# Optimization experiments

Measured on AMD Instinct MI355X. Metric: run time of the kernel, lower is better.

Reference implementation:

```python
import jax, jax.numpy as jnp
import numpy as np

N_EMBD = 1024
N_HEAD = 16
B, T = 8, 1024

def setup_inputs() -> dict:
    key = jax.random.key(0)
    ks = jax.random.split(key, 5)
    s = 0.02
    return {
        'x': jax.random.normal(ks[0], (B, T, N_EMBD), dtype=jnp.float32),
        'w_attn': jax.random.normal(ks[1], (N_EMBD, 3 * N_EMBD), dtype=jnp.float32) * s,
        'b_attn': jax.random.normal(ks[2], (3 * N_EMBD,), dtype=jnp.float32) * s,
        'w_proj': jax.random.normal(ks[3], (N_EMBD, N_EMBD), dtype=jnp.float32) * s,
        'b_proj': jax.random.normal(ks[4], (N_EMBD,), dtype=jnp.float32) * s,
    }

def reference(x, w_attn, b_attn, w_proj, b_proj):
    Bb, Tt, C = x.shape
    hd = C // N_HEAD  # head dim
    qkv = x @ w_attn + b_attn                      # [B,T,3C]
    q, k, v = jnp.split(qkv, 3, axis=2)
    # [B,T,C] -> [B,H,T,hd]
    def to_heads(t):
        return t.reshape(Bb, Tt, N_HEAD, hd).transpose(0, 2, 1, 3)
    q, k, v = to_heads(q), to_heads(k), to_heads(v)
    scale = 1.0 / jnp.sqrt(jnp.asarray(hd, dtype=x.dtype))
    att = jnp.einsum('bhqd,bhkd->bhqk', q, k) * scale  # [B,H,T,T]
    causal = jnp.tril(jnp.ones((Tt, Tt), dtype=bool))  # [T,T]
    att = jnp.where(causal[None, None, :, :], att, -jnp.inf)
    att = jax.nn.softmax(att, axis=-1)
    y = jnp.einsum('bhqk,bhkd->bhqd', att, v)          # [B,H,T,hd]
    y = y.transpose(0, 2, 1, 3).reshape(Bb, Tt, C)
    y = y @ w_proj + b_proj
    return y
```

## Files before the change

kernel.cpp:

```cpp
#include <hip/hip_runtime.h>
#include <stdint.h>

#define N_EMBD 1024
#define NHEAD  16
#define HDIM   64
#define BATCH  8
#define SEQ    1024
#define MROWS  (BATCH*SEQ)

typedef __bf16 bf16x8 __attribute__((ext_vector_type(8)));
typedef float  f32x4  __attribute__((ext_vector_type(4)));

__device__ inline unsigned short f2bf(float f) {
  uint32_t u = __float_as_uint(f);
  u += 0x7FFFu + ((u >> 16) & 1u);
  return (unsigned short)(u >> 16);
}

__device__ inline f32x4 mfma_bf16(bf16x8 a, bf16x8 b, f32x4 c) {
  return __builtin_amdgcn_mfma_f32_16x16x32_bf16(a, b, c, 0, 0, 0);
}

__device__ inline void gload_lds16(const unsigned short* g, unsigned short* l) {
  __builtin_amdgcn_global_load_lds(
      (const __attribute__((address_space(1))) void*)g,
      (__attribute__((address_space(3))) void*)l,
      16, 0, 0);
}

#define DSB __builtin_amdgcn_sched_barrier(0)
#define BARRIER __builtin_amdgcn_s_barrier()
#define VMC(n) asm volatile("s_waitcnt vmcnt(" #n ")" ::: "memory")
#define LGKM0 asm volatile("s_waitcnt lgkmcnt(0)" ::: "memory"); DSB

__global__ __launch_bounds__(256) void cast_f32_bf16(
    const float* __restrict__ in, unsigned short* __restrict__ out, int n) {
  int i = (blockIdx.x * 256 + threadIdx.x) * 4;
  if (i >= n) return;
  float4 v = *(const float4*)(in + i);
  ushort4 o;
  o.x = f2bf(v.x); o.y = f2bf(v.y); o.z = f2bf(v.z); o.w = f2bf(v.w);
  *(ushort4*)(out + i) = o;
}

__global__ __launch_bounds__(256) void transpose_cast2(
    const float* __restrict__ wa, unsigned short* __restrict__ oa,
    const float* __restrict__ wp, unsigned short* __restrict__ op) {
  __shared__ unsigned short tile[64 * 72];
  const int K = 1024;
  int bx = blockIdx.x;
  const float* in; unsigned short* out; int N;
  if (bx < 48) { in = wa; out = oa; N = 3072; }
  else         { in = wp; out = op; N = 1024; bx -= 48; }
  int k0 = blockIdx.y * 64, n0 = bx * 64;
  int t = threadIdx.x;
  {
    int col = (t & 15) * 4;
#pragma unroll
    for (int it = 0; it < 4; ++it) {
      int row = (t >> 4) + it * 16;
      float4 v = *(const float4*)(in + (size_t)(k0 + row) * N + n0 + col);
      ushort4 o;
      o.x = f2bf(v.x); o.y = f2bf(v.y); o.z = f2bf(v.z); o.w = f2bf(v.w);
      *(ushort4*)&tile[row * 72 + col] = o;
    }
  }
  __syncthreads();
  {
    int kcol = (t & 7) * 8;
#pragma unroll
    for (int it = 0; it < 2; ++it) {
      int nrow = (t >> 3) + it * 32;
      alignas(16) unsigned short tmp[8];
#pragma unroll
      for (int j = 0; j < 8; ++j) tmp[j] = tile[(kcol + j) * 72 + nrow];
      *(uint4*)(out + (size_t)(n0 + nrow) * K + k0 + kcol) = *(const uint4*)tmp;
    }
  }
}

#define GEMM98_BODY(A_, Bt_)                                                    \
  __shared__ unsigned short Asl[2][8192];                                       \
  __shared__ unsigned short Bsl[2][8192];                                       \
  const int tid = threadIdx.x;                                                  \
  const int l = tid & 63, w = tid >> 6;                                         \
  const int wr = w >> 1, wc = w & 1;                                            \
  const int g = l >> 4, fr = l & 15;                                            \
  f32x4 acc[4][4];                                                              \
  _Pragma("unroll") for (int i = 0; i < 4; ++i)                                 \
    _Pragma("unroll") for (int j = 0; j < 4; ++j)                               \
      _Pragma("unroll") for (int r = 0; r < 4; ++r) acc[i][j][r] = 0.0f;        \
  const int rr = tid >> 3;                                                      \
  const int cs = ((tid & 7) * 16) ^ ((rr & 7) << 4);                            \
  const char* srcA[4]; const char* srcB[4];                                     \
  _Pragma("unroll") for (int c = 0; c < 4; ++c) {                               \
    srcA[c] = (const char*)(A_) + (size_t)(m0 + c * 32 + rr) * 2048 + cs;       \
    srcB[c] = (const char*)(Bt_) + (size_t)(n0 + c * 32 + rr) * 2048 + cs;      \
  }                                                                             \
  const int ldso = tid * 8;                                         \
  const int arow = (wr * 64 + fr) * 128;                                        \
  const int brow = (wc * 64 + fr) * 128;                                        \
  int colk[2];                                                                  \
  colk[0] = (g * 16) ^ ((fr & 7) << 4);                                         \
  colk[1] = (64 + g * 16) ^ ((fr & 7) << 4);                                    \
  _Pragma("unroll") for (int c = 0; c < 4; ++c)                                 \
    gload_lds16((const unsigned short*)(srcA[c]), &Asl[0][ldso + c * 2048]);    \
  _Pragma("unroll") for (int c = 0; c < 4; ++c)                                 \
    gload_lds16((const unsigned short*)(srcB[c]), &Bsl[0][ldso + c * 2048]);    \
  _Pragma("unroll") for (int c = 0; c < 4; ++c)                                 \
    gload_lds16((const unsigned short*)(srcA[c] + 128), &Asl[1][ldso + c * 2048]);\
  _Pragma("unroll") for (int c = 0; c < 4; ++c)                                 \
    gload_lds16((const unsigned short*)(srcB[c] + 128), &Bsl[1][ldso + c * 2048]);\
  for (int kt = 0; kt < 16; ++kt) {                                             \
    const int cur = kt & 1;                                                     \
    if (kt < 15) { VMC(8); } else { VMC(0); }                                   \
    DSB; BARRIER; DSB;                                                          \
    _Pragma("unroll") for (int ks = 0; ks < 2; ++ks) {                          \
      bf16x8 av[4], bv[4];                                                      \
      _Pragma("unroll") for (int m = 0; m < 4; ++m)                             \
        av[m] = *(const bf16x8*)((const char*)&Asl[cur][0] + arow +             \
                                 m * 16 * 128 + colk[ks]);                      \
      _Pragma("unroll") for (int n = 0; n < 4; ++n)                             \
        bv[n] = *(const bf16x8*)((const char*)&Bsl[cur][0] + brow +             \
                                 n * 16 * 128 + colk[ks]);                      \
      _Pragma("unroll") for (int n = 0; n < 4; ++n)                             \
        _Pragma("unroll") for (int m = 0; m < 4; ++m)                           \
          acc[m][n] = mfma_bf16(av[m], bv[n], acc[m][n]);                       \
    }                                                                           \
    LGKM0; BARRIER; DSB;                                                        \
    if (kt < 14) {                                                              \
      const int ko = (kt + 2) * 128;                                            \
      _Pragma("unroll") for (int c = 0; c < 4; ++c)                             \
        gload_lds16((const unsigned short*)(srcA[c] + ko),                      \
                    &Asl[cur][ldso + c * 2048]);                                \
      _Pragma("unroll") for (int c = 0; c < 4; ++c)                             \
        gload_lds16((const unsigned short*)(srcB[c] + ko),                      \
                    &Bsl[cur][ldso + c * 2048]);                                \
    }                                                                           \
  }

__global__ __launch_bounds__(256) void gemm_qkv(
    const unsigned short* __restrict__ A, const unsigned short* __restrict__ Bt,
    const float* __restrict__ bias,
    unsigned short* __restrict__ Qo, unsigned short* __restrict__ Ko,
    unsigned short* __restrict__ VTo) {
  const int bid = blockIdx.x;
  const int xcd = bid & 7;
  const int local = bid >> 3;
  const int nchunk = local >> 6;
  const int rem = local & 63;
  const int m0 = (xcd * 8 + (rem >> 3)) * 128;
  const int n0 = (nchunk * 8 + (rem & 7)) * 128;
  GEMM98_BODY(A, Bt)
#pragma unroll
  for (int i = 0; i < 4; ++i) {
    int mb = m0 + wr * 64 + i * 16 + 4 * g;
    int bidx = mb >> 10;
    int t = mb & 1023;
#pragma unroll
    for (int j = 0; j < 4; ++j) {
      int n = n0 + wc * 64 + j * 16 + fr;
      float bv2 = bias[n];
      int part = n >> 10;
      int nn2 = n & 1023;
      int h = nn2 >> 6, d = nn2 & 63;
      if (part == 2) {
        alignas(8) unsigned short pk[4];
#pragma unroll
        for (int r = 0; r < 4; ++r) pk[r] = f2bf(acc[i][j][r] + bv2);
        *(ushort4*)&VTo[((size_t)(bidx * NHEAD + h) * HDIM + d) * SEQ + t] =
            *(const ushort4*)pk;
      } else {
        unsigned short* dst = (part == 0) ? Qo : Ko;
        float scl = (part == 0) ? 0.125f : 1.0f;
        size_t base = ((size_t)(bidx * NHEAD + h) * SEQ + t) * HDIM + d;
#pragma unroll
        for (int r = 0; r < 4; ++r)
          dst[base + (size_t)r * HDIM] = f2bf((acc[i][j][r] + bv2) * scl);
      }
    }
  }
}

__global__ __launch_bounds__(256) void gemm_proj(
    const unsigned short* __restrict__ A, const unsigned short* __restrict__ Bt,
    const float* __restrict__ bias, float* __restrict__ Out) {
  const int bid = blockIdx.x;
  const int xcd = bid & 7;
  const int local = bid >> 3;
  const int m0 = (xcd * 8 + (local >> 3)) * 128;
  const int n0 = (local & 7) * 128;
  GEMM98_BODY(A, Bt)
#pragma unroll
  for (int i = 0; i < 4; ++i) {
    int mb = m0 + wr * 64 + i * 16 + 4 * g;
#pragma unroll
    for (int j = 0; j < 4; ++j) {
      int n = n0 + wc * 64 + j * 16 + fr;
      float bv2 = bias[n];
#pragma unroll
      for (int r = 0; r < 4; ++r)
        Out[(size_t)(mb + r) * N_EMBD + n] = acc[i][j][r] + bv2;
    }
  }
}

__global__ __launch_bounds__(256) void attn_kernel(
    const unsigned short* __restrict__ Q, const unsigned short* __restrict__ Kv,
    const unsigned short* __restrict__ VT, unsigned short* __restrict__ Y) {
  __shared__ unsigned short Kt[2][4096];
  __shared__ unsigned short Vt[2][4096];
  __shared__ unsigned short p_lds[4 * 32 * 72];
  __shared__ float smx[4][32];
  int tid = threadIdx.x, l = tid & 63, w = tid >> 6;
  int bid = blockIdx.x;
  int swz = (bid & 7) * 64 + (bid >> 3);
  int bh = swz >> 2;
  int pairIdx = swz & 3;
  int b = bh >> 4, h = bh & 15;
  const unsigned short* Qb = Q + (size_t)bh * SEQ * HDIM;
  const char* Kc = (const char*)(Kv + (size_t)bh * SEQ * HDIM);
  const char* Vc = (const char*)(VT + (size_t)bh * HDIM * SEQ);
  unsigned short* pw = &p_lds[w * 32 * 72];
  const int g = l >> 4;
  const int fr = l & 15;

  const int P0 = tid * 16, P1 = tid * 16 + 4096;
  const int r0 = P0 >> 7, r1 = P1 >> 7;
  const int s0 = (P0 & 127) ^ ((r0 & 7) << 4);
  const int s1 = (P1 & 127) ^ ((r1 & 7) << 4);
  const char* Kg0 = Kc + r0 * 128 + s0;
  const char* Kg1 = Kc + r1 * 128 + s1;
  const char* Vg0 = Vc + (size_t)r0 * 2048 + s0;
  const char* Vg1 = Vc + (size_t)r1 * 2048 + s1;

  const int bc = (16 * g) ^ ((l & 7) << 4);

  for (int part = 0; part < 2; ++part) {
    const int qt = (part == 0) ? pairIdx : 7 - pairIdx;
    const int q0 = qt * 128;
    const int wq = q0 + w * 32;

    bf16x8 aq[2][2];
#pragma unroll
    for (int i = 0; i < 2; ++i)
#pragma unroll
      for (int ik = 0; ik < 2; ++ik)
        aq[i][ik] = *(const bf16x8*)&Qb[(size_t)(wq + i * 16 + fr) * HDIM + ik * 32 + 8 * g];

    float mrun[2], lpart[2];
    mrun[0] = mrun[1] = 0.0f;
    lpart[0] = lpart[1] = 0.0f;
    f32x4 acc_o[2][4];
#pragma unroll
    for (int i = 0; i < 2; ++i)
#pragma unroll
      for (int jd = 0; jd < 4; ++jd)
#pragma unroll
        for (int r = 0; r < 4; ++r) acc_o[i][jd][r] = 0.0f;

    const int n_it = (q0 + 128) >> 6;

    gload_lds16((const unsigned short*)(Kg0), &Kt[0][P0 >> 1]);
    gload_lds16((const unsigned short*)(Kg1), &Kt[0][P1 >> 1]);
    gload_lds16((const unsigned short*)(Vg0), &Vt[0][P0 >> 1]);
    gload_lds16((const unsigned short*)(Vg1), &Vt[0][P1 >> 1]);

    for (int it = 0; it < n_it; ++it) {
      const int kv0 = it << 6;
      const int cur = it & 1;
      if (it + 1 < n_it) {
        const int nx = kv0 + 64;
        gload_lds16((const unsigned short*)(Kg0 + nx * 128), &Kt[cur ^ 1][P0 >> 1]);
        gload_lds16((const unsigned short*)(Kg1 + nx * 128), &Kt[cur ^ 1][P1 >> 1]);
        gload_lds16((const unsigned short*)(Vg0 + nx * 2),   &Vt[cur ^ 1][P0 >> 1]);
        gload_lds16((const unsigned short*)(Vg1 + nx * 2),   &Vt[cur ^ 1][P1 >> 1]);
        VMC(4);
      } else {
        VMC(0);
      }
      DSB; BARRIER; DSB;

      const char* Kbuf = (const char*)Kt[cur];
      const char* Vbuf = (const char*)Vt[cur];

      f32x4 s2[2][4];
#pragma unroll
      for (int i = 0; i < 2; ++i)
#pragma unroll
        for (int j = 0; j < 4; ++j)
#pragma unroll
          for (int r = 0; r < 4; ++r) s2[i][j][r] = 0.0f;

      __builtin_amdgcn_s_setprio(1);
#pragma unroll
      for (int ik = 0; ik < 2; ++ik) {
#pragma unroll
        for (int j = 0; j < 4; ++j) {
          bf16x8 bk = *(const bf16x8*)(Kbuf + (j * 16 + fr) * 128 + (bc ^ (ik << 6)));
#pragma unroll
          for (int i = 0; i < 2; ++i) s2[i][j] = mfma_bf16(bk, aq[i][ik], s2[i][j]);
        }
      }
      __builtin_amdgcn_s_setprio(0);

      bool need_mask = (kv0 + 63) > wq;
      if (need_mask) {
#pragma unroll
        for (int i = 0; i < 2; ++i) {
          int q = wq + i * 16 + fr;
#pragma unroll
          for (int j = 0; j < 4; ++j)
#pragma unroll
            for (int r = 0; r < 4; ++r) {
              int kv = kv0 + j * 16 + 4 * g + r;
              if (kv > q) s2[i][j][r] = -3.0e38f;
            }
        }
      }

      float pmloc[2];
#pragma unroll
      for (int i = 0; i < 2; ++i) {
        float m01 = fmaxf(fmaxf(s2[i][0][0], s2[i][0][1]), fmaxf(s2[i][0][2], s2[i][0][3]));
        float m11 = fmaxf(fmaxf(s2[i][1][0], s2[i][1][1]), fmaxf(s2[i][1][2], s2[i][1][3]));
        float m21 = fmaxf(fmaxf(s2[i][2][0], s2[i][2][1]), fmaxf(s2[i][2][2], s2[i][2][3]));
        float m31 = fmaxf(fmaxf(s2[i][3][0], s2[i][3][1]), fmaxf(s2[i][3][2], s2[i][3][3]));
        pmloc[i] = fmaxf(fmaxf(m01, m11), fmaxf(m21, m31));
      }
      bool ok = (pmloc[0] <= mrun[0] + 8.0f) && (pmloc[1] <= mrun[1] + 8.0f);
      if (!__all(ok)) {
#pragma unroll
        for (int i = 0; i < 2; ++i) {
          float mm = pmloc[i];
          mm = fmaxf(mm, __shfl_xor(mm, 16, 64));
          mm = fmaxf(mm, __shfl_xor(mm, 32, 64));
          float mn = fmaxf(mrun[i], mm);
          float sc = __expf(mrun[i] - mn);
          mrun[i] = mn;
          lpart[i] *= sc;
          if (g == 0) smx[w][i * 16 + fr] = sc;
        }
        asm volatile("s_waitcnt lgkmcnt(0)" ::: "memory");
#pragma unroll
        for (int i = 0; i < 2; ++i)
#pragma unroll
          for (int r = 0; r < 4; ++r) {
            float sc = smx[w][i * 16 + 4 * g + r];
#pragma unroll
            for (int jd = 0; jd < 4; ++jd) acc_o[i][jd][r] *= sc;
          }
      }

#pragma unroll
      for (int i = 0; i < 2; ++i) {
#pragma unroll
        for (int j = 0; j < 4; ++j) {
          float p0 = __expf(s2[i][j][0] - mrun[i]);
          float p1 = __expf(s2[i][j][1] - mrun[i]);
          float p2 = __expf(s2[i][j][2] - mrun[i]);
          float p3 = __expf(s2[i][j][3] - mrun[i]);
          lpart[i] += (p0 + p1) + (p2 + p3);
          uint2 pk2;
          asm("v_cvt_pk_bf16_f32 %0, %1, %2" : "=v"(pk2.x) : "v"(p0), "v"(p1));
          asm("v_cvt_pk_bf16_f32 %0, %1, %2" : "=v"(pk2.y) : "v"(p2), "v"(p3));
          *(uint2*)&pw[(i * 16 + fr) * 72 + j * 16 + 4 * g] = pk2;
        }
      }

      __builtin_amdgcn_s_setprio(1);
#pragma unroll
      for (int ik2 = 0; ik2 < 2; ++ik2) {
        bf16x8 ap[2];
#pragma unroll
        for (int i = 0; i < 2; ++i)
          ap[i] = *(const bf16x8*)&pw[(i * 16 + fr) * 72 + ik2 * 32 + 8 * g];
#pragma unroll
        for (int jd = 0; jd < 4; ++jd) {
          bf16x8 bv = *(const bf16x8*)(Vbuf + (jd * 16 + fr) * 128 + (bc ^ (ik2 << 6)));
#pragma unroll
          for (int i = 0; i < 2; ++i) acc_o[i][jd] = mfma_bf16(ap[i], bv, acc_o[i][jd]);
        }
      }
      __builtin_amdgcn_s_setprio(0);

      asm volatile("s_waitcnt lgkmcnt(0)" ::: "memory");
      DSB; BARRIER; DSB;
    }

#pragma unroll
    for (int i = 0; i < 2; ++i) {
      float t = lpart[i];
      t += __shfl_xor(t, 16, 64);
      t += __shfl_xor(t, 32, 64);
      if (g == 0) smx[w][i * 16 + fr] = t;
    }
    asm volatile("s_waitcnt lgkmcnt(0)" ::: "memory");
#pragma unroll
    for (int i = 0; i < 2; ++i)
#pragma unroll
      for (int r = 0; r < 4; ++r) {
        float inv = 1.0f / smx[w][i * 16 + 4 * g + r];
        int q = wq + i * 16 + 4 * g + r;
#pragma unroll
        for (int jd = 0; jd < 4; ++jd)
          Y[((size_t)b * SEQ + q) * N_EMBD + h * HDIM + jd * 16 + fr] =
              f2bf(acc_o[i][jd][r] * inv);
      }
  }
}

extern "C" void kernel_launch(void* const* d_in, const int* in_sizes, int n_in,
                              void* d_out, int out_size, void* d_ws, size_t ws_size,
                              hipStream_t stream) {
  (void)in_sizes; (void)n_in; (void)out_size; (void)ws_size;
  const float* x      = (const float*)d_in[0];
  const float* w_attn = (const float*)d_in[1];
  const float* b_attn = (const float*)d_in[2];
  const float* w_proj = (const float*)d_in[3];
  const float* b_proj = (const float*)d_in[4];
  float* out = (float*)d_out;

  char* ws = (char*)d_ws;
  size_t off = 0;
  auto carve = [&](size_t bytes) -> char* {
    char* p = ws + off;
    off += (bytes + 255) & ~(size_t)255;
    return p;
  };
  unsigned short* xb     = (unsigned short*)carve((size_t)MROWS * N_EMBD * 2);
  unsigned short* wTattn = (unsigned short*)carve((size_t)3 * N_EMBD * N_EMBD * 2);
  unsigned short* wTproj = (unsigned short*)carve((size_t)N_EMBD * N_EMBD * 2);
  unsigned short* Qb     = (unsigned short*)carve((size_t)MROWS * N_EMBD * 2);
  unsigned short* Kb     = (unsigned short*)carve((size_t)MROWS * N_EMBD * 2);
  unsigned short* VTb    = (unsigned short*)carve((size_t)MROWS * N_EMBD * 2);
  unsigned short* Yb     = (unsigned short*)carve((size_t)MROWS * N_EMBD * 2);
  carve(4096);

  cast_f32_bf16<<<dim3(MROWS * N_EMBD / 1024), 256, 0, stream>>>(x, xb, MROWS * N_EMBD);
  transpose_cast2<<<dim3(64, 16), 256, 0, stream>>>(w_attn, wTattn, w_proj, wTproj);
  gemm_qkv<<<dim3(1536), 256, 0, stream>>>(xb, wTattn, b_attn, Qb, Kb, VTb);
  attn_kernel<<<dim3(512), 256, 0, stream>>>(Qb, Kb, VTb, Yb);
  gemm_proj<<<dim3(512), 256, 0, stream>>>(Yb, wTproj, b_proj, out);
}
```

Before: 141.6 us.

## Merge prep kernels, stage QKV epilogue through LDS, fold log2e into Q

```diff
diff --git a/kernel.cpp b/kernel.cpp
--- a/kernel.cpp
+++ b/kernel.cpp
@@ -33,27 +33,29 @@
 #define VMC(n) asm volatile("s_waitcnt vmcnt(" #n ")" ::: "memory")
 #define LGKM0 asm volatile("s_waitcnt lgkmcnt(0)" ::: "memory"); DSB
 
-__global__ __launch_bounds__(256) void cast_f32_bf16(
-    const float* __restrict__ in, unsigned short* __restrict__ out, int n) {
-  int i = (blockIdx.x * 256 + threadIdx.x) * 4;
-  if (i >= n) return;
-  float4 v = *(const float4*)(in + i);
-  ushort4 o;
-  o.x = f2bf(v.x); o.y = f2bf(v.y); o.z = f2bf(v.z); o.w = f2bf(v.w);
-  *(ushort4*)(out + i) = o;
-}
-
-__global__ __launch_bounds__(256) void transpose_cast2(
+__global__ __launch_bounds__(256) void prep_kernel(
+    const float* __restrict__ x, unsigned short* __restrict__ xb,
     const float* __restrict__ wa, unsigned short* __restrict__ oa,
     const float* __restrict__ wp, unsigned short* __restrict__ op) {
+  int bid = blockIdx.x;
+  int t = threadIdx.x;
+  if (bid < 8192) {
+    int i = (bid * 256 + t) * 4;
+    float4 v = *(const float4*)(x + i);
+    ushort4 o;
+    o.x = f2bf(v.x); o.y = f2bf(v.y); o.z = f2bf(v.z); o.w = f2bf(v.w);
+    *(ushort4*)(xb + i) = o;
+    return;
+  }
   __shared__ unsigned short tile[64 * 72];
+  int idx = bid - 8192;
+  int bx = idx & 63;
+  int ky = idx >> 6;
   const int K = 1024;
-  int bx = blockIdx.x;
   const float* in; unsigned short* out; int N;
   if (bx < 48) { in = wa; out = oa; N = 3072; }
   else         { in = wp; out = op; N = 1024; bx -= 48; }
-  int k0 = blockIdx.y * 64, n0 = bx * 64;
-  int t = threadIdx.x;
+  int k0 = ky * 64, n0 = bx * 64;
   {
     int col = (t & 15) * 4;
 #pragma unroll
@@ -152,32 +154,52 @@
   const int m0 = (xcd * 8 + (rem >> 3)) * 128;
   const int n0 = (nchunk * 8 + (rem & 7)) * 128;
   GEMM98_BODY(A, Bt)
-#pragma unroll
-  for (int i = 0; i < 4; ++i) {
-    int mb = m0 + wr * 64 + i * 16 + 4 * g;
-    int bidx = mb >> 10;
-    int t = mb & 1023;
-#pragma unroll
-    for (int j = 0; j < 4; ++j) {
-      int n = n0 + wc * 64 + j * 16 + fr;
-      float bv2 = bias[n];
-      int part = n >> 10;
-      int nn2 = n & 1023;
-      int h = nn2 >> 6, d = nn2 & 63;
-      if (part == 2) {
-        alignas(8) unsigned short pk[4];
-#pragma unroll
-        for (int r = 0; r < 4; ++r) pk[r] = f2bf(acc[i][j][r] + bv2);
-        *(ushort4*)&VTo[((size_t)(bidx * NHEAD + h) * HDIM + d) * SEQ + t] =
-            *(const ushort4*)pk;
-      } else {
-        unsigned short* dst = (part == 0) ? Qo : Ko;
-        float scl = (part == 0) ? 0.125f : 1.0f;
-        size_t base = ((size_t)(bidx * NHEAD + h) * SEQ + t) * HDIM + d;
+  const int nw0 = n0 + wc * 64;
+  const int part = nw0 >> 10;
+  const int h = (nw0 & 1023) >> 6;
+  const int mw0 = m0 + wr * 64;
+  const int bidx = mw0 >> 10;
+  const int t0 = mw0 & 1023;
+  unsigned short* stg = (w < 3) ? ((unsigned short*)Asl + w * 4608)
+                                : ((unsigned short*)Bsl);
+  float bvj[4];
+#pragma unroll
+  for (int j = 0; j < 4; ++j) bvj[j] = bias[nw0 + j * 16 + fr];
+  if (part < 2) {
+    const float scl = (part == 0) ? 0.18033688f : 1.0f;
+#pragma unroll
+    for (int i = 0; i < 4; ++i)
+#pragma unroll
+      for (int j = 0; j < 4; ++j)
 #pragma unroll
         for (int r = 0; r < 4; ++r)
-          dst[base + (size_t)r * HDIM] = f2bf((acc[i][j][r] + bv2) * scl);
-      }
+          stg[(i * 16 + 4 * g + r) * 72 + j * 16 + fr] =
+              f2bf((acc[i][j][r] + bvj[j]) * scl);
+    LGKM0;
+    unsigned short* dst = (part == 0) ? Qo : Ko;
+    size_t base = ((size_t)(bidx * NHEAD + h) * SEQ + t0) * HDIM + (l & 7) * 8;
+#pragma unroll
+    for (int it = 0; it < 8; ++it) {
+      int row = (l >> 3) + it * 8;
+      uint4 v = *(const uint4*)&stg[row * 72 + (l & 7) * 8];
+      *(uint4*)&dst[base + (size_t)row * HDIM] = v;
+    }
+  } else {
+#pragma unroll
+    for (int i = 0; i < 4; ++i)
+#pragma unroll
+      for (int j = 0; j < 4; ++j)
+#pragma unroll
+        for (int r = 0; r < 4; ++r)
+          stg[(j * 16 + fr) * 72 + i * 16 + 4 * g + r] =
+              f2bf(acc[i][j][r] + bvj[j]);
+    LGKM0;
+    size_t base = ((size_t)(bidx * NHEAD + h) * HDIM) * SEQ + t0 + (l & 7) * 8;
+#pragma unroll
+    for (int it = 0; it < 8; ++it) {
+      int row = (l >> 3) + it * 8;
+      uint4 v = *(const uint4*)&stg[row * 72 + (l & 7) * 8];
+      *(uint4*)&VTo[base + (size_t)row * SEQ] = v;
     }
   }
 }
@@ -328,7 +350,7 @@
         float m31 = fmaxf(fmaxf(s2[i][3][0], s2[i][3][1]), fmaxf(s2[i][3][2], s2[i][3][3]));
         pmloc[i] = fmaxf(fmaxf(m01, m11), fmaxf(m21, m31));
       }
-      bool ok = (pmloc[0] <= mrun[0] + 8.0f) && (pmloc[1] <= mrun[1] + 8.0f);
+      bool ok = (pmloc[0] <= mrun[0] + 11.5409f) && (pmloc[1] <= mrun[1] + 11.5409f);
       if (!__all(ok)) {
 #pragma unroll
         for (int i = 0; i < 2; ++i) {
@@ -336,7 +358,7 @@
           mm = fmaxf(mm, __shfl_xor(mm, 16, 64));
           mm = fmaxf(mm, __shfl_xor(mm, 32, 64));
           float mn = fmaxf(mrun[i], mm);
-          float sc = __expf(mrun[i] - mn);
+          float sc = exp2f(mrun[i] - mn);
           mrun[i] = mn;
           lpart[i] *= sc;
           if (g == 0) smx[w][i * 16 + fr] = sc;
@@ -356,10 +378,10 @@
       for (int i = 0; i < 2; ++i) {
 #pragma unroll
         for (int j = 0; j < 4; ++j) {
-          float p0 = __expf(s2[i][j][0] - mrun[i]);
-          float p1 = __expf(s2[i][j][1] - mrun[i]);
-          float p2 = __expf(s2[i][j][2] - mrun[i]);
-          float p3 = __expf(s2[i][j][3] - mrun[i]);
+          float p0 = exp2f(s2[i][j][0] - mrun[i]);
+          float p1 = exp2f(s2[i][j][1] - mrun[i]);
+          float p2 = exp2f(s2[i][j][2] - mrun[i]);
+          float p3 = exp2f(s2[i][j][3] - mrun[i]);
           lpart[i] += (p0 + p1) + (p2 + p3);
           uint2 pk2;
           asm("v_cvt_pk_bf16_f32 %0, %1, %2" : "=v"(pk2.x) : "v"(p0), "v"(p1));
@@ -437,8 +459,7 @@
   unsigned short* Yb     = (unsigned short*)carve((size_t)MROWS * N_EMBD * 2);
   carve(4096);
 
-  cast_f32_bf16<<<dim3(MROWS * N_EMBD / 1024), 256, 0, stream>>>(x, xb, MROWS * N_EMBD);
-  transpose_cast2<<<dim3(64, 16), 256, 0, stream>>>(w_attn, wTattn, w_proj, wTproj);
+  prep_kernel<<<dim3(8192 + 1024), 256, 0, stream>>>(x, xb, w_attn, wTattn, w_proj, wTproj);
   gemm_qkv<<<dim3(1536), 256, 0, stream>>>(xb, wTattn, b_attn, Qb, Kb, VTb);
   attn_kernel<<<dim3(512), 256, 0, stream>>>(Qb, Kb, VTb, Yb);
   gemm_proj<<<dim3(512), 256, 0, stream>>>(Yb, wTproj, b_proj, out);
```

Measured after the change: 144.9 us. +2.3%, slower.
